# Optimization experiments

Measured on AMD Instinct MI355X. Metric: run time of the kernel, lower is better.

## Reference

```python
import jax, jax.numpy as jnp
import numpy as np

B, S, DM = 1, 4096, 2048
H, HD = 16, 128
TS = 16          # tile_size
TOPK = 16        # anchor tiles per query
NUM_TILES = S // TS


def setup_inputs() -> dict:
    key = jax.random.key(0)
    ks = jax.random.split(key, 7)
    x = jax.random.normal(ks[0], (B, S, DM), jnp.float32)
    Wq = jax.random.normal(ks[1], (DM, H * HD), jnp.float32) * 0.02
    Wk = jax.random.normal(ks[2], (DM, H * HD), jnp.float32) * 0.02
    Wv = jax.random.normal(ks[3], (DM, H * HD), jnp.float32) * 0.02
    Wo = jax.random.normal(ks[4], (H * HD, DM), jnp.float32) * 0.02
    # RoPE angles: pos * inv_freq, shape [S, HD//2] (= freqs_cis angle)
    inv_freq = 1.0 / (10000.0 ** (np.arange(0, HD, 2, dtype=np.float32) / HD))
    freqs = jnp.asarray(np.arange(S, dtype=np.float32)[:, None] * inv_freq[None, :])
    anchor_indices = jax.random.randint(ks[5], (B, H, S, TOPK), 0, NUM_TILES).astype(jnp.int32)
    return {"x": x, "Wq": Wq, "Wk": Wk, "Wv": Wv, "Wo": Wo,
            "freqs": freqs, "anchor_indices": anchor_indices}


def _rotate_half(z):
    half = z.shape[-1] // 2
    return jnp.concatenate([-z[..., half:], z[..., :half]], axis=-1)


def reference(x, Wq, Wk, Wv, Wo, freqs, anchor_indices):
    b, s, _ = x.shape
    num_tiles = s // TS
    # QKV projections -> [B, H, S, HD]
    q = (x @ Wq).reshape(b, s, H, HD).transpose(0, 2, 1, 3)
    k = (x @ Wk).reshape(b, s, H, HD).transpose(0, 2, 1, 3)
    v = (x @ Wv).reshape(b, s, H, HD).transpose(0, 2, 1, 3)
    # RoPE (half-split / rotate_half convention), float32
    cos = jnp.cos(freqs)[None, None, :s, :]
    sin = jnp.sin(freqs)[None, None, :s, :]
    cos_full = jnp.concatenate([cos, cos], axis=-1)
    sin_full = jnp.concatenate([sin, sin], axis=-1)
    q = q * cos_full + _rotate_half(q) * sin_full
    k = k * cos_full + _rotate_half(k) * sin_full
    # Per-query tile indices: anchor tiles + local tile
    local_tiles = (jnp.arange(s) // TS).astype(jnp.int32)
    local = jnp.broadcast_to(local_tiles[None, None, :, None], (b, H, s, 1))
    tiles = jnp.concatenate([anchor_indices, local], axis=-1)  # [B,H,S,K+1]
    # Representative query per tile (last token of each query tile)
    tile_repr = jnp.arange(TS - 1, s, TS)
    tile_sel = tiles[:, :, tile_repr, :]                        # [B,H,T,K+1]
    # Expand tile indices to token indices
    offsets = jnp.arange(TS)
    token_idx = tile_sel[..., None] * TS + offsets              # [B,H,T,K+1,TS]
    sparse_len = tile_sel.shape[-1] * TS
    flat_idx = jnp.clip(token_idx.reshape(b, H, num_tiles, sparse_len), 0, s - 1)
    # Gather sparse K/V per (batch, head, query-tile)
    k_flat = k.reshape(b * H, s, HD)
    v_flat = v.reshape(b * H, s, HD)
    idx_flat = flat_idx.reshape(b * H, num_tiles, sparse_len)
    k_sparse = jax.vmap(lambda kv, idx: kv[idx])(k_flat, idx_flat)
    v_sparse = jax.vmap(lambda kv, idx: kv[idx])(v_flat, idx_flat)
    k_sparse = k_sparse.reshape(b, H, num_tiles, sparse_len, HD)
    v_sparse = v_sparse.reshape(b, H, num_tiles, sparse_len, HD)
    # Block-sparse attention per tile
    q_tiled = q.reshape(b, H, num_tiles, TS, HD)
    logits = jnp.einsum('bhtqd,bhtkd->bhtqk', q_tiled, k_sparse) / jnp.sqrt(HD)
    q_pos = jnp.arange(s).reshape(num_tiles, TS)
    future_mask = flat_idx[:, :, :, None, :] > q_pos[None, None, :, :, None]
    logits = jnp.where(future_mask, -1e10, logits)
    weights = jax.nn.softmax(logits, axis=-1)
    all_masked = jnp.all(future_mask, axis=-1, keepdims=True)
    weights = jnp.where(all_masked, 0.0, weights)
    weights = jnp.where(jnp.isnan(weights), 0.0, weights)
    out = jnp.einsum('bhtqk,bhtkd->bhtqd', weights, v_sparse)
    out = out.reshape(b, H, s, HD).transpose(0, 2, 1, 3).reshape(b, s, H * HD)
    return out @ Wo
```

## Files before the change

### kernel.cpp

```cpp
#include <hip/hip_runtime.h>

typedef unsigned short u16;
typedef unsigned int u32;
typedef __attribute__((ext_vector_type(8))) short bf16x8;
typedef __attribute__((ext_vector_type(4))) float f32x4;

__device__ __forceinline__ u16 f2bf(float f) {
  union { float f; u32 u; } v; v.f = f;
  u32 u = v.u;
  return (u16)((u + 0x7FFFu + ((u >> 16) & 1u)) >> 16);
}
__device__ __forceinline__ float bf2f(u16 s) {
  union { u32 u; float f; } v; v.u = ((u32)s) << 16;
  return v.f;
}

__device__ __forceinline__ void async16(const void* g, void* l) {
  __builtin_amdgcn_global_load_lds(
      (__attribute__((address_space(1))) void*)g,
      (__attribute__((address_space(3))) void*)l, 16, 0, 0);
}

__global__ void cast4_kernel(const float* __restrict__ in, u16* __restrict__ out, int n4) {
  int i = blockIdx.x * 256 + threadIdx.x;
  if (i < n4) {
    float4 v = ((const float4*)in)[i];
    ushort4 o;
    o.x = f2bf(v.x); o.y = f2bf(v.y); o.z = f2bf(v.z); o.w = f2bf(v.w);
    ((ushort4*)out)[i] = o;
  }
}

__global__ void transpose_cast4_kernel(const float* __restrict__ W0, const float* __restrict__ W1,
                                       const float* __restrict__ W2, const float* __restrict__ W3,
                                       u16* __restrict__ O0, u16* __restrict__ O1,
                                       u16* __restrict__ O2, u16* __restrict__ O3) {
  const int R = 2048, C = 2048;
  const int z = blockIdx.z;
  const float* in = z == 0 ? W0 : z == 1 ? W1 : z == 2 ? W2 : W3;
  u16* out = z == 0 ? O0 : z == 1 ? O1 : z == 2 ? O2 : O3;
  __shared__ float tile[32][33];
  int c0 = blockIdx.x * 32, r0 = blockIdx.y * 32;
  int tx = threadIdx.x, ty = threadIdx.y;
#pragma unroll
  for (int i = ty; i < 32; i += 8) tile[i][tx] = in[(size_t)(r0 + i) * C + c0 + tx];
  __syncthreads();
#pragma unroll
  for (int i = ty; i < 32; i += 8)
    out[(size_t)(c0 + i) * R + r0 + tx] = f2bf(tile[tx][i]);
}

__global__ void trig_kernel(const float* __restrict__ freqs, float* __restrict__ ct,
                            float* __restrict__ st, int n) {
  int i = blockIdx.x * 256 + threadIdx.x;
  if (i < n) { float f = freqs[i]; ct[i] = cosf(f); st[i] = sinf(f); }
}

__global__ void rope_kernel(u16* __restrict__ q, const u16* __restrict__ k,
                            u16* __restrict__ Kp,
                            const float* __restrict__ ct, const float* __restrict__ st) {
  int i = blockIdx.x * 256 + threadIdx.x;
  int dp = (i & 31) * 2;
  int hh = (i >> 5) & 15;
  int s  = i >> 9;
  float c0 = ct[s * 64 + dp], c1 = ct[s * 64 + dp + 1];
  float s0 = st[s * 64 + dp], s1 = st[s * 64 + dp + 1];
  size_t base = (size_t)s * 2048 + hh * 128 + dp;
  {
    u32 lo = *(u32*)(q + base);
    u32 hi = *(u32*)(q + base + 64);
    float a0 = bf2f((u16)lo), a1 = bf2f((u16)(lo >> 16));
    float b0 = bf2f((u16)hi), b1 = bf2f((u16)(hi >> 16));
    u32 nlo = (u32)f2bf(a0 * c0 - b0 * s0) | ((u32)f2bf(a1 * c1 - b1 * s1) << 16);
    u32 nhi = (u32)f2bf(b0 * c0 + a0 * s0) | ((u32)f2bf(b1 * c1 + a1 * s1) << 16);
    *(u32*)(q + base) = nlo;
    *(u32*)(q + base + 64) = nhi;
  }
  {
    u32 lo = *(const u32*)(k + base);
    u32 hi = *(const u32*)(k + base + 64);
    float a0 = bf2f((u16)lo), a1 = bf2f((u16)(lo >> 16));
    float b0 = bf2f((u16)hi), b1 = bf2f((u16)(hi >> 16));
    u32 nlo = (u32)f2bf(a0 * c0 - b0 * s0) | ((u32)f2bf(a1 * c1 - b1 * s1) << 16);
    u32 nhi = (u32)f2bf(b0 * c0 + a0 * s0) | ((u32)f2bf(b1 * c1 + a1 * s1) << 16);
    size_t kpb = ((size_t)hh * 4096 + s) * 128 + dp;
    *(u32*)(Kp + kpb) = nlo;
    *(u32*)(Kp + kpb + 64) = nhi;
  }
}

__global__ void repack_v_kernel(const u16* __restrict__ Vin, u16* __restrict__ VT2) {
  const int h = blockIdx.y;
  const int s0 = blockIdx.x * 64;
  const int tid = threadIdx.x;
  __shared__ u16 lv[64][132];
#pragma unroll
  for (int i = 0; i < 16; ++i) {
    int idx = i * 256 + tid;
    int r = idx >> 6;
    int d2 = idx & 63;
    u32 vv = ((const u32*)Vin)[(size_t)(s0 + r) * 1024 + h * 64 + d2];
    *(u32*)(&lv[r][d2 * 2]) = vv;
  }
  __syncthreads();
#pragma unroll
  for (int i = 0; i < 16; ++i) {
    int idx = i * 256 + tid;
    int k2 = idx & 7;
    int d  = (idx >> 3) & 127;
    int tl = idx >> 10;
    u32 lo = lv[tl * 16 + k2 * 2][d];
    u32 hi = lv[tl * 16 + k2 * 2 + 1][d];
    ((u32*)VT2)[(((size_t)h * 256 + blockIdx.x * 4 + tl) * 128 + d) * 8 + k2] = lo | (hi << 16);
  }
}

template <int MODE>
__launch_bounds__(256, 2)
__global__ void gemm128_kernel(const u16* __restrict__ A, const u16* __restrict__ Bt,
                               void* __restrict__ C, u16* __restrict__ D1, u16* __restrict__ D2,
                               int M, int N, int K) {
  __shared__ __align__(16) u16 As[128 * 64];
  __shared__ __align__(16) u16 Bs[128 * 64];
  const int tid  = threadIdx.x;
  const int lane = tid & 63;
  const int wave = tid >> 6;
  const int wr = wave >> 1, wc = wave & 1;
  const int brow = blockIdx.y * 128;
  const int bcol = blockIdx.x * 128;

  int a_goff[4], b_goff[4], l_off[4];
#pragma unroll
  for (int i = 0; i < 4; ++i) {
    int p = (wave * 4 + i) * 1024 + lane * 16;
    int row = p >> 7;
    int colb = (p & 127) ^ ((row & 7) << 4);
    a_goff[i] = (brow + row) * K + (colb >> 1);
    b_goff[i] = (bcol + row) * K + (colb >> 1);
    l_off[i] = p;
  }

  f32x4 acc[4][4];
#pragma unroll
  for (int m = 0; m < 4; ++m)
#pragma unroll
    for (int n = 0; n < 4; ++n) acc[m][n] = (f32x4){0.f, 0.f, 0.f, 0.f};

  for (int k0 = 0; k0 < K; k0 += 64) {
#pragma unroll
    for (int i = 0; i < 4; ++i) {
      async16(A + a_goff[i] + k0, (char*)As + l_off[i]);
      async16(Bt + b_goff[i] + k0, (char*)Bs + l_off[i]);
    }
    __syncthreads();
#pragma unroll
    for (int kk = 0; kk < 2; ++kk) {
      bf16x8 af[4], bfr[4];
#pragma unroll
      for (int m = 0; m < 4; ++m) {
        int row = wr * 64 + m * 16 + (lane & 15);
        int byte = (row << 7) + ((kk * 64 + ((lane >> 4) << 4)) ^ ((row & 7) << 4));
        af[m] = *(const bf16x8*)((const char*)As + byte);
      }
#pragma unroll
      for (int n = 0; n < 4; ++n) {
        int row = wc * 64 + n * 16 + (lane & 15);
        int byte = (row << 7) + ((kk * 64 + ((lane >> 4) << 4)) ^ ((row & 7) << 4));
        bfr[n] = *(const bf16x8*)((const char*)Bs + byte);
      }
#pragma unroll
      for (int m = 0; m < 4; ++m)
#pragma unroll
        for (int n = 0; n < 4; ++n)
          acc[m][n] = __builtin_amdgcn_mfma_f32_16x16x32_bf16(af[m], bfr[n], acc[m][n], 0, 0, 0);
    }
    __syncthreads();
  }

  const int r0 = brow + wr * 64;
  const int c0 = bcol + wc * 64;
  if (MODE == 2) {
    const int sel = bcol >> 11;
    u16* dst = sel == 0 ? (u16*)C : sel == 1 ? D1 : D2;
    const int c0l = (bcol & 2047) + wc * 64;
#pragma unroll
    for (int m = 0; m < 4; ++m)
#pragma unroll
      for (int n = 0; n < 4; ++n)
#pragma unroll
        for (int r = 0; r < 4; ++r) {
          int rr = r0 + m * 16 + ((lane >> 4) << 2) + r;
          int cc = c0l + n * 16 + (lane & 15);
          dst[(size_t)rr * 2048 + cc] = f2bf(acc[m][n][r]);
        }
  } else {
#pragma unroll
    for (int m = 0; m < 4; ++m)
#pragma unroll
      for (int n = 0; n < 4; ++n)
#pragma unroll
        for (int r = 0; r < 4; ++r) {
          int rr = r0 + m * 16 + ((lane >> 4) << 2) + r;
          int cc = c0 + n * 16 + (lane & 15);
          if (MODE == 1) ((u16*)C)[(size_t)rr * N + cc] = f2bf(acc[m][n][r]);
          else           ((float*)C)[(size_t)rr * N + cc] = acc[m][n][r];
        }
  }
}

__launch_bounds__(256, 4)
__global__ void attn_kernel(const u16* __restrict__ Q, const u16* __restrict__ Kp,
                            const u16* __restrict__ VT2, const int* __restrict__ anchors,
                            u16* __restrict__ Out) {
  const int t = blockIdx.x;
  const int h = blockIdx.y;
  __shared__ int tiles[20];
  __shared__ float lg[16][292];
  __shared__ __align__(16) u16 w_lds[16][296];
  const int tid  = threadIdx.x;
  const int lane = tid & 63;
  const int wave = tid >> 6;
  const int g = lane >> 4;
  const int c = lane & 15;

  if (tid < 16) tiles[tid] = anchors[(size_t)((h << 12) + (t * 16 + 15)) * 16 + tid];
  if (tid == 16) tiles[16] = t;
  if (tid >= 17 && tid < 20) tiles[tid] = 0;
  __syncthreads();

  {
    const u16* qbase = Q + (size_t)(t * 16 + c) * 2048 + h * 128 + g * 8;
    bf16x8 qf[4];
#pragma unroll
    for (int ks = 0; ks < 4; ++ks) qf[ks] = *(const bf16x8*)(qbase + ks * 32);

    int tok_[5];
    const u16* kb_[5];
#pragma unroll
    for (int i = 0; i < 5; ++i) {
      int j = wave + 4 * i;
      tok_[i] = tiles[j] * 16 + c;
      kb_[i] = Kp + ((size_t)h * 4096 + tok_[i]) * 128 + g * 8;
    }
    bf16x8 kfp[2][4];
#pragma unroll
    for (int ks = 0; ks < 4; ++ks) kfp[0][ks] = *(const bf16x8*)(kb_[0] + ks * 32);
#pragma unroll
    for (int i = 0; i < 5; ++i) {
      if (i < 4) {
#pragma unroll
        for (int ks = 0; ks < 4; ++ks)
          kfp[(i + 1) & 1][ks] = *(const bf16x8*)(kb_[i + 1] + ks * 32);
      }
      f32x4 a = (f32x4){0.f, 0.f, 0.f, 0.f};
#pragma unroll
      for (int ks = 0; ks < 4; ++ks)
        a = __builtin_amdgcn_mfma_f32_16x16x32_bf16(qf[ks], kfp[i & 1][ks], a, 0, 0, 0);
      int j = wave + 4 * i;
      if (j < 17) {
#pragma unroll
        for (int r = 0; r < 4; ++r) {
          int qrow = g * 4 + r;
          float vv = a[r] * 0.088388347648318447f;
          if (tok_[i] > t * 16 + qrow) vv = -1e10f;
          lg[qrow][j * 16 + c] = vv;
        }
      }
    }
  }
  __syncthreads();

  {
    const int r = tid >> 4, cc = tid & 15;
    float vals[17];
    float mx = -3.0e38f;
#pragma unroll
    for (int i = 0; i < 17; ++i) { vals[i] = lg[r][i * 16 + cc]; mx = fmaxf(mx, vals[i]); }
#pragma unroll
    for (int d = 1; d < 16; d <<= 1) mx = fmaxf(mx, __shfl_xor(mx, d, 64));
    float sum = 0.f;
#pragma unroll
    for (int i = 0; i < 17; ++i) { vals[i] = __expf(vals[i] - mx); sum += vals[i]; }
#pragma unroll
    for (int d = 1; d < 16; d <<= 1) sum += __shfl_xor(sum, d, 64);
    float inv = sum > 0.f ? 1.0f / sum : 0.f;
#pragma unroll
    for (int i = 0; i < 17; ++i) w_lds[r][i * 16 + cc] = f2bf(vals[i] * inv);
    w_lds[r][272 + cc] = 0;
  }
  __syncthreads();

  {
    f32x4 o0 = (f32x4){0.f, 0.f, 0.f, 0.f}, o1 = o0;
    const int d0 = wave * 32;
    const size_t hb = (size_t)h * 256;
    const int keyin = (g & 1) * 8;
    const u16* vb_[9];
#pragma unroll
    for (int ks = 0; ks < 9; ++ks) vb_[ks] = VT2 + (hb + tiles[2 * ks + (g >> 1)]) * 2048;
    bf16x8 pb0[2], pb1[2];
    pb0[0] = *(const bf16x8*)(vb_[0] + (d0 + c) * 16 + keyin);
    pb1[0] = *(const bf16x8*)(vb_[0] + (d0 + 16 + c) * 16 + keyin);
#pragma unroll
    for (int ks = 0; ks < 9; ++ks) {
      if (ks < 8) {
        pb0[(ks + 1) & 1] = *(const bf16x8*)(vb_[ks + 1] + (d0 + c) * 16 + keyin);
        pb1[(ks + 1) & 1] = *(const bf16x8*)(vb_[ks + 1] + (d0 + 16 + c) * 16 + keyin);
      }
      bf16x8 af = *(const bf16x8*)(&w_lds[c][ks * 32 + g * 8]);
      o0 = __builtin_amdgcn_mfma_f32_16x16x32_bf16(af, pb0[ks & 1], o0, 0, 0, 0);
      o1 = __builtin_amdgcn_mfma_f32_16x16x32_bf16(af, pb1[ks & 1], o1, 0, 0, 0);
    }
#pragma unroll
    for (int r = 0; r < 4; ++r) {
      int qrow = g * 4 + r;
      size_t base = (size_t)(t * 16 + qrow) * 2048 + h * 128;
      Out[base + d0 + c]      = f2bf(o0[r]);
      Out[base + d0 + 16 + c] = f2bf(o1[r]);
    }
  }
}

extern "C" void kernel_launch(void* const* d_in, const int* in_sizes, int n_in,
                              void* d_out, int out_size, void* d_ws, size_t ws_size,
                              hipStream_t stream) {
  (void)in_sizes; (void)n_in; (void)out_size; (void)ws_size;
  const float* x      = (const float*)d_in[0];
  const float* Wq     = (const float*)d_in[1];
  const float* Wk     = (const float*)d_in[2];
  const float* Wv     = (const float*)d_in[3];
  const float* Wo     = (const float*)d_in[4];
  const float* freqs  = (const float*)d_in[5];
  const int* anchors  = (const int*)d_in[6];
  float* out = (float*)d_out;

  char* ws = (char*)d_ws;
  const size_t MB = 1024 * 1024;
  u16* xbf   = (u16*)(ws + 0);
  u16* wqkvT = (u16*)(ws + 16 * MB);
  u16* woT   = (u16*)(ws + 40 * MB);
  u16* qbf   = (u16*)(ws + 48 * MB);
  u16* kbf   = (u16*)(ws + 64 * MB);
  u16* vbf   = (u16*)(ws + 80 * MB);
  u16* attnb = (u16*)(ws + 0);
  u16* Kp    = (u16*)(ws + 16 * MB);
  float* ct  = (float*)(ws + 32 * MB);
  float* st  = (float*)(ws + 33 * MB);
  u16* VT2   = (u16*)(ws + 64 * MB);

  cast4_kernel<<<8192, 256, 0, stream>>>(x, xbf, 2097152);
  dim3 tb(32, 8), tg4(64, 64, 4);
  transpose_cast4_kernel<<<tg4, tb, 0, stream>>>(
      Wq, Wk, Wv, Wo,
      wqkvT, wqkvT + (size_t)8 * MB / 2, wqkvT + (size_t)16 * MB / 2, woT);

  gemm128_kernel<2><<<dim3(48, 32), 256, 0, stream>>>(xbf, wqkvT, qbf, kbf, vbf,
                                                      4096, 6144, 2048);
  trig_kernel<<<1024, 256, 0, stream>>>(freqs, ct, st, 262144);
  rope_kernel<<<8192, 256, 0, stream>>>(qbf, kbf, Kp, ct, st);
  repack_v_kernel<<<dim3(64, 16), 256, 0, stream>>>(vbf, VT2);
  attn_kernel<<<dim3(256, 16), 256, 0, stream>>>(qbf, Kp, VT2, anchors, attnb);
  gemm128_kernel<0><<<dim3(16, 32), 256, 0, stream>>>(attnb, woT, out, nullptr, nullptr,
                                                      4096, 2048, 2048);
}
```

Measured before the change: 251.9 us.

## Double-buffer GEMM LDS tiles, remap blocks across XCDs, shrink attention LDS

The GEMM kernel now keeps two LDS buffers per operand and issues the async global-to-LDS loads for the next K-tile before computing the current one. This hides load latency behind the MFMA work and leaves a single barrier per iteration. It also remaps block IDs so neighbouring tiles are spread across XCDs for better L2 reuse, and it raises wave priority around the MFMA bursts. The attention kernel writes its bf16 softmax weights in place over the float logits buffer, which cuts LDS use so the launch bound can rise to 6 blocks per CU. The trade-offs are that the GEMM LDS footprint doubles, and the block remap assumes the block count is divisible by 8.

```diff
diff --git a/kernel.cpp b/kernel.cpp
--- a/kernel.cpp
+++ b/kernel.cpp
@@ -120,14 +120,21 @@
 __global__ void gemm128_kernel(const u16* __restrict__ A, const u16* __restrict__ Bt,
                                void* __restrict__ C, u16* __restrict__ D1, u16* __restrict__ D2,
                                int M, int N, int K) {
-  __shared__ __align__(16) u16 As[128 * 64];
-  __shared__ __align__(16) u16 Bs[128 * 64];
+  __shared__ __align__(16) u16 As[2][128 * 64];
+  __shared__ __align__(16) u16 Bs[2][128 * 64];
   const int tid  = threadIdx.x;
   const int lane = tid & 63;
   const int wave = tid >> 6;
   const int wr = wave >> 1, wc = wave & 1;
-  const int brow = blockIdx.y * 128;
-  const int bcol = blockIdx.x * 128;
+
+  const int nbx = gridDim.x, nby = gridDim.y;
+  const int nwg = nbx * nby;
+  const int bid = blockIdx.y * nbx + blockIdx.x;
+  const int sbid = (bid & 7) * (nwg >> 3) + (bid >> 3);
+  const int bx = sbid / nby;
+  const int by = sbid % nby;
+  const int brow = by * 128;
+  const int bcol = bx * 128;
 
   int a_goff[4], b_goff[4], l_off[4];
 #pragma unroll
@@ -146,13 +153,23 @@
 #pragma unroll
     for (int n = 0; n < 4; ++n) acc[m][n] = (f32x4){0.f, 0.f, 0.f, 0.f};
 
-  for (int k0 = 0; k0 < K; k0 += 64) {
+  auto stage = [&](int bufi, int k0) {
 #pragma unroll
     for (int i = 0; i < 4; ++i) {
-      async16(A + a_goff[i] + k0, (char*)As + l_off[i]);
-      async16(Bt + b_goff[i] + k0, (char*)Bs + l_off[i]);
-    }
-    __syncthreads();
+      async16(A + a_goff[i] + k0, (char*)As[bufi] + l_off[i]);
+      async16(Bt + b_goff[i] + k0, (char*)Bs[bufi] + l_off[i]);
+    }
+  };
+
+  const int nt = K >> 6;
+  stage(0, 0);
+  asm volatile("s_waitcnt vmcnt(0)" ::: "memory");
+  __builtin_amdgcn_s_barrier();
+  __builtin_amdgcn_sched_barrier(0);
+
+  for (int t = 0; t < nt; ++t) {
+    const int b = t & 1;
+    if (t + 1 < nt) stage(b ^ 1, (t + 1) << 6);
 #pragma unroll
     for (int kk = 0; kk < 2; ++kk) {
       bf16x8 af[4], bfr[4];
@@ -160,21 +177,25 @@
       for (int m = 0; m < 4; ++m) {
         int row = wr * 64 + m * 16 + (lane & 15);
         int byte = (row << 7) + ((kk * 64 + ((lane >> 4) << 4)) ^ ((row & 7) << 4));
-        af[m] = *(const bf16x8*)((const char*)As + byte);
+        af[m] = *(const bf16x8*)((const char*)As[b] + byte);
       }
 #pragma unroll
       for (int n = 0; n < 4; ++n) {
         int row = wc * 64 + n * 16 + (lane & 15);
         int byte = (row << 7) + ((kk * 64 + ((lane >> 4) << 4)) ^ ((row & 7) << 4));
-        bfr[n] = *(const bf16x8*)((const char*)Bs + byte);
-      }
+        bfr[n] = *(const bf16x8*)((const char*)Bs[b] + byte);
+      }
+      __builtin_amdgcn_s_setprio(1);
 #pragma unroll
       for (int m = 0; m < 4; ++m)
 #pragma unroll
         for (int n = 0; n < 4; ++n)
           acc[m][n] = __builtin_amdgcn_mfma_f32_16x16x32_bf16(af[m], bfr[n], acc[m][n], 0, 0, 0);
-    }
-    __syncthreads();
+      __builtin_amdgcn_s_setprio(0);
+    }
+    asm volatile("s_waitcnt vmcnt(0)" ::: "memory");
+    __builtin_amdgcn_s_barrier();
+    __builtin_amdgcn_sched_barrier(0);
   }
 
   const int r0 = brow + wr * 64;
@@ -208,15 +229,14 @@
   }
 }
 
-__launch_bounds__(256, 4)
+__launch_bounds__(256, 6)
 __global__ void attn_kernel(const u16* __restrict__ Q, const u16* __restrict__ Kp,
                             const u16* __restrict__ VT2, const int* __restrict__ anchors,
                             u16* __restrict__ Out) {
   const int t = blockIdx.x;
   const int h = blockIdx.y;
   __shared__ int tiles[20];
-  __shared__ float lg[16][292];
-  __shared__ __align__(16) u16 w_lds[16][296];
+  __shared__ __align__(16) float lg[16][292];
   const int tid  = threadIdx.x;
   const int lane = tid & 63;
   const int wave = tid >> 6;
@@ -284,9 +304,10 @@
 #pragma unroll
     for (int d = 1; d < 16; d <<= 1) sum += __shfl_xor(sum, d, 64);
     float inv = sum > 0.f ? 1.0f / sum : 0.f;
-#pragma unroll
-    for (int i = 0; i < 17; ++i) w_lds[r][i * 16 + cc] = f2bf(vals[i] * inv);
-    w_lds[r][272 + cc] = 0;
+    u16* wrow = (u16*)&lg[r][0];
+#pragma unroll
+    for (int i = 0; i < 17; ++i) wrow[i * 16 + cc] = f2bf(vals[i] * inv);
+    wrow[272 + cc] = 0;
   }
   __syncthreads();
 
@@ -295,6 +316,7 @@
     const int d0 = wave * 32;
     const size_t hb = (size_t)h * 256;
     const int keyin = (g & 1) * 8;
+    const u16* wrow = (const u16*)&lg[c][0];
     const u16* vb_[9];
 #pragma unroll
     for (int ks = 0; ks < 9; ++ks) vb_[ks] = VT2 + (hb + tiles[2 * ks + (g >> 1)]) * 2048;
@@ -307,7 +329,7 @@
         pb0[(ks + 1) & 1] = *(const bf16x8*)(vb_[ks + 1] + (d0 + c) * 16 + keyin);
         pb1[(ks + 1) & 1] = *(const bf16x8*)(vb_[ks + 1] + (d0 + 16 + c) * 16 + keyin);
       }
-      bf16x8 af = *(const bf16x8*)(&w_lds[c][ks * 32 + g * 8]);
+      bf16x8 af = *(const bf16x8*)(wrow + ks * 32 + g * 8);
       o0 = __builtin_amdgcn_mfma_f32_16x16x32_bf16(af, pb0[ks & 1], o0, 0, 0, 0);
       o1 = __builtin_amdgcn_mfma_f32_16x16x32_bf16(af, pb1[ks & 1], o1, 0, 0, 0);
     }
```

Measured after the change: 260.2 us. 1.03x slower.
